# Kernel optimization log

Hardware: AMD Instinct MI355X
Metric: run time of the kernel (lower is better)

Reference implementation:

```python
import jax, jax.numpy as jnp
import numpy as np

B, S, H, F, E = 2, 2048, 1024, 4096, 8  # batch, seq, hidden, ffn, num_experts


def setup_inputs() -> dict:
    key = jax.random.key(0)
    ks = jax.random.split(key, 4)
    x = jax.random.normal(ks[0], (B, S, H), dtype=jnp.float32)
    w_router = jax.random.normal(ks[1], (H, E), dtype=jnp.float32) * 0.02
    w1 = jax.random.normal(ks[2], (E, H, F), dtype=jnp.float32) * 0.02
    b1 = jnp.zeros((E, F), dtype=jnp.float32)
    w2 = jax.random.normal(ks[3], (E, F, H), dtype=jnp.float32) * 0.02
    b2 = jnp.zeros((E, H), dtype=jnp.float32)
    return {"x": x, "w_router": w_router, "w1": w1, "b1": b1, "w2": w2, "b2": b2}


def reference(x, w_router, w1, b1, w2, b2):
    """Top-1 MoE layer: route -> per-expert FFN -> weighted combine.

    Faithful to ExpertParallelWrapper._process_moe_layer on a single group:
    router picks one expert per token with a routing weight; tokens are
    dispatched to experts (here expressed as a static mask over the fixed
    expert set), processed by the expert FFN, and scatter-combined back
    weighted by the routing probability.
    """
    Bs, Ss, Hs = x.shape
    n_experts = w1.shape[0]
    # Router: per-token logits -> softmax -> top-1 expert + weight
    logits = jnp.einsum('bsh,he->bse', x, w_router)          # [B,S,E]
    probs = jax.nn.softmax(logits, axis=-1)
    sel = jnp.argmax(probs, axis=-1)                          # [B,S] selected expert
    wgt = jnp.take_along_axis(probs, sel[..., None], axis=-1)[..., 0]  # [B,S]

    xt = x.reshape(-1, Hs)        # [T,H] flat tokens
    sel_t = sel.reshape(-1)       # [T]
    wgt_t = wgt.reshape(-1)       # [T]

    out = jnp.zeros_like(xt)
    # Static loop over the small fixed expert set (dispatch/combine via mask).
    for e in range(n_experts):
        h = jax.nn.relu(xt @ w1[e] + b1[e])   # [T,F]
        y = h @ w2[e] + b2[e]                 # [T,H]
        m = (sel_t == e).astype(xt.dtype) * wgt_t
        out = out + m[:, None] * y
    return out.reshape(Bs, Ss, Hs)
```

## Files before the change

### kernel.cpp

```cpp
#include <hip/hip_runtime.h>
#include <math.h>

#define T_TOK 4096
#define H_DIM 1024
#define F_DIM 4096
#define E_NUM 8
#define BK 64

typedef __attribute__((ext_vector_type(8))) short bhalf8_t;
typedef __attribute__((ext_vector_type(8))) unsigned short ushort8_t;
typedef __attribute__((ext_vector_type(4))) float f32x4_t;

__device__ __forceinline__ unsigned short f2bf(float f) {
  unsigned int u = __float_as_uint(f);
  return (unsigned short)((u + 0x7fffu + ((u >> 16) & 1u)) >> 16);
}

__device__ __forceinline__ void gload16(const void* g, void* l) {
  __builtin_amdgcn_global_load_lds(
      (const __attribute__((address_space(1))) unsigned int*)g,
      (__attribute__((address_space(3))) unsigned int*)l, 16, 0, 0);
}

__global__ void k_init(int* counts) {
  if (threadIdx.x < E_NUM) counts[threadIdx.x] = 0;
}

__global__ __launch_bounds__(256) void k_router(const float* __restrict__ x,
                                                const float* __restrict__ wr,
                                                int* __restrict__ sel, float* __restrict__ wgt,
                                                int* __restrict__ counts) {
  const int t = blockIdx.x * 4 + (threadIdx.x >> 6);
  const int lane = threadIdx.x & 63;
  const float* xr = x + (size_t)t * H_DIM;
  double acc[E_NUM] = {0, 0, 0, 0, 0, 0, 0, 0};
  for (int h = lane; h < H_DIM; h += 64) {
    const double xv = (double)xr[h];
    const float* w = wr + (size_t)h * E_NUM;
#pragma unroll
    for (int e = 0; e < E_NUM; ++e) acc[e] += xv * (double)w[e];
  }
#pragma unroll
  for (int e = 0; e < E_NUM; ++e) {
#pragma unroll
    for (int off = 32; off > 0; off >>= 1) acc[e] += __shfl_down(acc[e], off, 64);
  }
  if (lane == 0) {
    double m = acc[0];
    int a = 0;
#pragma unroll
    for (int e = 1; e < E_NUM; ++e)
      if (acc[e] > m) { m = acc[e]; a = e; }
    double s = 0.0;
#pragma unroll
    for (int e = 0; e < E_NUM; ++e) s += exp(acc[e] - m);
    sel[t] = a;
    wgt[t] = (float)(1.0 / s);
    atomicAdd(&counts[a], 1);
  }
}

__global__ void k_prefix(const int* __restrict__ counts, int* __restrict__ offs,
                         int* __restrict__ cursors) {
  if (threadIdx.x == 0 && blockIdx.x == 0) {
    int s = 0;
    for (int e = 0; e < E_NUM; ++e) {
      offs[e] = s;
      cursors[e] = s;
      s += counts[e];
    }
    offs[E_NUM] = s;
  }
}

__global__ void k_scatter(const float* __restrict__ x, const int* __restrict__ sel,
                          const float* __restrict__ wgt, int* __restrict__ cursors,
                          int* __restrict__ s2t, float* __restrict__ wgtS,
                          unsigned short* __restrict__ Xs) {
  const int t = blockIdx.x;
  __shared__ int sslot;
  if (threadIdx.x == 0) {
    const int slot = atomicAdd(&cursors[sel[t]], 1);
    sslot = slot;
    s2t[slot] = t;
    wgtS[slot] = wgt[t];
  }
  __syncthreads();
  const int slot = sslot;
  const float4 v = reinterpret_cast<const float4*>(x + (size_t)t * H_DIM)[threadIdx.x];
  ushort4 o;
  o.x = f2bf(v.x); o.y = f2bf(v.y); o.z = f2bf(v.z); o.w = f2bf(v.w);
  reinterpret_cast<ushort4*>(Xs + (size_t)slot * H_DIM)[threadIdx.x] = o;
}

__global__ __launch_bounds__(256) void k_transpose(const float* __restrict__ in,
                                                   unsigned short* __restrict__ out,
                                                   int K, int N) {
  const int e = blockIdx.z;
  const int n0 = blockIdx.x * 64;
  const int k0 = blockIdx.y * 64;
  __shared__ float tile[64][65];
  const float* src = in + (size_t)e * K * N;
  unsigned short* dst = out + (size_t)e * N * K;
  const int l = threadIdx.x;
  const int lr = l >> 4;
  const int lc = (l & 15) * 4;
#pragma unroll
  for (int i = 0; i < 64; i += 16) {
    const float4 v = *reinterpret_cast<const float4*>(&src[(size_t)(k0 + lr + i) * N + n0 + lc]);
    tile[lr + i][lc] = v.x;
    tile[lr + i][lc + 1] = v.y;
    tile[lr + i][lc + 2] = v.z;
    tile[lr + i][lc + 3] = v.w;
  }
  __syncthreads();
  const int kk = (l & 7) * 8;
  const int nr = l >> 3;
#pragma unroll
  for (int i = 0; i < 64; i += 32) {
    const int n = nr + i;
    ushort8_t o;
#pragma unroll
    for (int j = 0; j < 8; ++j) o[j] = f2bf(tile[kk + j][n]);
    *reinterpret_cast<ushort8_t*>(&dst[(size_t)(n0 + n) * K + k0 + kk]) = o;
  }
}

__global__ __launch_bounds__(256, 4) void k_ffn1(const unsigned short* __restrict__ Xs,
                                                 const unsigned short* __restrict__ Wt,
                                                 const float* __restrict__ b1,
                                                 unsigned short* __restrict__ Hws,
                                                 const int* __restrict__ offs) {
  const int e = blockIdx.z;
  const int off = offs[e];
  const int cnt = offs[e + 1] - off;
  const int m0 = blockIdx.y * 128;
  if (m0 >= cnt) return;
  const int n0 = blockIdx.x * 128;
  const int msize = cnt - m0;

  __shared__ short lA[128 * BK];
  __shared__ short lB[128 * BK];

  const int tid = threadIdx.x;
  const int lane = tid & 63;
  const int wv = tid >> 6;
  const int wm = (wv >> 1) * 64;
  const int wn = (wv & 1) * 64;

  const int sRow = lane >> 3;
  const int cc = lane & 7;
  const int gch = cc ^ sRow;

  const unsigned short* Abase = Xs + (size_t)off * H_DIM;
  const unsigned short* Bbase = Wt + (size_t)e * F_DIM * H_DIM + (size_t)n0 * H_DIM;

  f32x4_t acc[4][4];
#pragma unroll
  for (int i = 0; i < 4; ++i)
#pragma unroll
    for (int j = 0; j < 4; ++j) acc[i][j] = (f32x4_t){0.f, 0.f, 0.f, 0.f};

  const int q = lane >> 4;
  const int r16 = lane & 15;
  const int sw = r16 & 7;

  for (int k0 = 0; k0 < H_DIM; k0 += BK) {
    __syncthreads();
#pragma unroll
    for (int i = 0; i < 4; ++i) {
      const int g = wv * 4 + i;
      const int row = g * 8 + sRow;
      const int ar = (row < msize) ? row : 0;
      gload16(Abase + (size_t)(m0 + ar) * H_DIM + k0 + gch * 8, &lA[g * 8 * BK]);
      gload16(Bbase + (size_t)row * H_DIM + k0 + gch * 8, &lB[g * 8 * BK]);
    }
    __syncthreads();

#pragma unroll
    for (int step = 0; step < 2; ++step) {
      const int slot = (step * 4 + q) ^ sw;
      bhalf8_t af[4], bf[4];
#pragma unroll
      for (int mi = 0; mi < 4; ++mi)
        af[mi] = *reinterpret_cast<const bhalf8_t*>(&lA[(wm + mi * 16 + r16) * BK + slot * 8]);
#pragma unroll
      for (int ni = 0; ni < 4; ++ni)
        bf[ni] = *reinterpret_cast<const bhalf8_t*>(&lB[(wn + ni * 16 + r16) * BK + slot * 8]);
#pragma unroll
      for (int mi = 0; mi < 4; ++mi)
#pragma unroll
        for (int ni = 0; ni < 4; ++ni)
          acc[mi][ni] = __builtin_amdgcn_mfma_f32_16x16x32_bf16(af[mi], bf[ni], acc[mi][ni], 0, 0, 0);
    }
  }

  const int c = lane & 15;
#pragma unroll
  for (int ni = 0; ni < 4; ++ni) {
    const int col = n0 + wn + ni * 16 + c;
    const float bias = b1[e * F_DIM + col];
#pragma unroll
    for (int mi = 0; mi < 4; ++mi) {
      const int rbase = wm + mi * 16 + q * 4;
#pragma unroll
      for (int r = 0; r < 4; ++r) {
        const int row = rbase + r;
        if (row < msize) {
          float v = acc[mi][ni][r] + bias;
          v = fmaxf(v, 0.0f);
          Hws[(size_t)(off + m0 + row) * F_DIM + col] = f2bf(v);
        }
      }
    }
  }
}

__global__ __launch_bounds__(256, 4) void k_ffn2(const unsigned short* __restrict__ Hws,
                                                 const unsigned short* __restrict__ Wt,
                                                 const float* __restrict__ b2,
                                                 const int* __restrict__ offs,
                                                 const int* __restrict__ s2t,
                                                 const float* __restrict__ wgtS,
                                                 float* __restrict__ out) {
  const int e = blockIdx.z;
  const int off = offs[e];
  const int cnt = offs[e + 1] - off;
  const int m0 = blockIdx.y * 128;
  if (m0 >= cnt) return;
  const int n0 = blockIdx.x * 128;
  const int msize = cnt - m0;

  __shared__ short lA[128 * BK];
  __shared__ short lB[128 * BK];

  const int tid = threadIdx.x;
  const int lane = tid & 63;
  const int wv = tid >> 6;
  const int wm = (wv >> 1) * 64;
  const int wn = (wv & 1) * 64;

  const int sRow = lane >> 3;
  const int cc = lane & 7;
  const int gch = cc ^ sRow;

  const unsigned short* Abase = Hws + (size_t)off * F_DIM;
  const unsigned short* Bbase = Wt + (size_t)e * H_DIM * F_DIM + (size_t)n0 * F_DIM;

  f32x4_t acc[4][4];
#pragma unroll
  for (int i = 0; i < 4; ++i)
#pragma unroll
    for (int j = 0; j < 4; ++j) acc[i][j] = (f32x4_t){0.f, 0.f, 0.f, 0.f};

  const int q = lane >> 4;
  const int r16 = lane & 15;
  const int sw = r16 & 7;

  for (int k0 = 0; k0 < F_DIM; k0 += BK) {
    __syncthreads();
#pragma unroll
    for (int i = 0; i < 4; ++i) {
      const int g = wv * 4 + i;
      const int row = g * 8 + sRow;
      const int ar = (row < msize) ? row : 0;
      gload16(Abase + (size_t)(m0 + ar) * F_DIM + k0 + gch * 8, &lA[g * 8 * BK]);
      gload16(Bbase + (size_t)row * F_DIM + k0 + gch * 8, &lB[g * 8 * BK]);
    }
    __syncthreads();

#pragma unroll
    for (int step = 0; step < 2; ++step) {
      const int slot = (step * 4 + q) ^ sw;
      bhalf8_t af[4], bf[4];
#pragma unroll
      for (int mi = 0; mi < 4; ++mi)
        af[mi] = *reinterpret_cast<const bhalf8_t*>(&lA[(wm + mi * 16 + r16) * BK + slot * 8]);
#pragma unroll
      for (int ni = 0; ni < 4; ++ni)
        bf[ni] = *reinterpret_cast<const bhalf8_t*>(&lB[(wn + ni * 16 + r16) * BK + slot * 8]);
#pragma unroll
      for (int mi = 0; mi < 4; ++mi)
#pragma unroll
        for (int ni = 0; ni < 4; ++ni)
          acc[mi][ni] = __builtin_amdgcn_mfma_f32_16x16x32_bf16(af[mi], bf[ni], acc[mi][ni], 0, 0, 0);
    }
  }

  const int c = lane & 15;
#pragma unroll
  for (int mi = 0; mi < 4; ++mi) {
    const int rbase = wm + mi * 16 + q * 4;
#pragma unroll
    for (int r = 0; r < 4; ++r) {
      const int row = rbase + r;
      if (row >= msize) continue;
      const int srow = off + m0 + row;
      const int tok = s2t[srow];
      const float w = wgtS[srow];
      float* orow = out + (size_t)tok * H_DIM;
#pragma unroll
      for (int ni = 0; ni < 4; ++ni) {
        const int col = n0 + wn + ni * 16 + c;
        orow[col] = w * (acc[mi][ni][r] + b2[e * H_DIM + col]);
      }
    }
  }
}

extern "C" void kernel_launch(void* const* d_in, const int* in_sizes, int n_in,
                              void* d_out, int out_size, void* d_ws, size_t ws_size,
                              hipStream_t stream) {
  const float* x  = (const float*)d_in[0];
  const float* wr = (const float*)d_in[1];
  const float* w1 = (const float*)d_in[2];
  const float* b1 = (const float*)d_in[3];
  const float* w2 = (const float*)d_in[4];
  const float* b2 = (const float*)d_in[5];
  float* out = (float*)d_out;

  char* ws = (char*)d_ws;
  unsigned short* WT  = (unsigned short*)(ws);
  unsigned short* XS  = (unsigned short*)(ws + 67108864);
  unsigned short* HWS = (unsigned short*)(ws + 67108864 + 8388608);
  char* ctrl = ws + 67108864 + 8388608 + 33554432;
  int*   sel     = (int*)(ctrl);
  int*   s2t     = (int*)(ctrl + 16384);
  float* wgt     = (float*)(ctrl + 32768);
  float* wgtS    = (float*)(ctrl + 49152);
  int*   counts  = (int*)(ctrl + 65536);
  int*   offs    = (int*)(ctrl + 65536 + 64);
  int*   cursors = (int*)(ctrl + 65536 + 128);

  k_init<<<1, 64, 0, stream>>>(counts);
  k_router<<<T_TOK / 4, 256, 0, stream>>>(x, wr, sel, wgt, counts);
  k_prefix<<<1, 1, 0, stream>>>(counts, offs, cursors);
  k_scatter<<<T_TOK, 256, 0, stream>>>(x, sel, wgt, cursors, s2t, wgtS, XS);

  k_transpose<<<dim3(F_DIM / 64, H_DIM / 64, E_NUM), 256, 0, stream>>>(w1, WT, H_DIM, F_DIM);
  k_ffn1<<<dim3(F_DIM / 128, T_TOK / 128, E_NUM), 256, 0, stream>>>(XS, WT, b1, HWS, offs);

  k_transpose<<<dim3(H_DIM / 64, F_DIM / 64, E_NUM), 256, 0, stream>>>(w2, WT, F_DIM, H_DIM);
  k_ffn2<<<dim3(H_DIM / 128, T_TOK / 128, E_NUM), 256, 0, stream>>>(HWS, WT, b2, offs, s2t, wgtS, out);
}
```

Before: 579.9 us.

## Split-K the second expert GEMM and narrow FFN1 tiles for more blocks

The second expert GEMM is split four ways along the F dimension. Each split writes fp32 partial sums to a workspace buffer, and a new reduce kernel adds them, applies bias and routing weight, and scatters rows back to token order. The first GEMM's N tile drops from 128 to 64 to double block count. Both changes aim to fill the GPU better when per-expert token counts are small. The cost is extra global traffic for partials plus a reduce launch, and lower arithmetic intensity per FFN1 block. Split-K runs only when the workspace is large enough.

Result: faster. 551.9 us (-4.8%).

```diff
diff --git a/kernel.cpp b/kernel.cpp
--- a/kernel.cpp
+++ b/kernel.cpp
@@ -6,6 +6,7 @@
 #define F_DIM 4096
 #define E_NUM 8
 #define BK 64
+#define KSPLIT 4
 
 typedef __attribute__((ext_vector_type(8))) short bhalf8_t;
 typedef __attribute__((ext_vector_type(8))) unsigned short ushort8_t;
@@ -76,14 +77,16 @@
 __global__ void k_scatter(const float* __restrict__ x, const int* __restrict__ sel,
                           const float* __restrict__ wgt, int* __restrict__ cursors,
                           int* __restrict__ s2t, float* __restrict__ wgtS,
-                          unsigned short* __restrict__ Xs) {
+                          int* __restrict__ eS, unsigned short* __restrict__ Xs) {
   const int t = blockIdx.x;
   __shared__ int sslot;
   if (threadIdx.x == 0) {
-    const int slot = atomicAdd(&cursors[sel[t]], 1);
+    const int e = sel[t];
+    const int slot = atomicAdd(&cursors[e], 1);
     sslot = slot;
     s2t[slot] = t;
     wgtS[slot] = wgt[t];
+    eS[slot] = e;
   }
   __syncthreads();
   const int slot = sslot;
@@ -136,17 +139,17 @@
   const int cnt = offs[e + 1] - off;
   const int m0 = blockIdx.y * 128;
   if (m0 >= cnt) return;
-  const int n0 = blockIdx.x * 128;
+  const int n0 = blockIdx.x * 64;
   const int msize = cnt - m0;
 
   __shared__ short lA[128 * BK];
-  __shared__ short lB[128 * BK];
+  __shared__ short lB[64 * BK];
 
   const int tid = threadIdx.x;
   const int lane = tid & 63;
   const int wv = tid >> 6;
   const int wm = (wv >> 1) * 64;
-  const int wn = (wv & 1) * 64;
+  const int wn = (wv & 1) * 32;
 
   const int sRow = lane >> 3;
   const int cc = lane & 7;
@@ -155,11 +158,11 @@
   const unsigned short* Abase = Xs + (size_t)off * H_DIM;
   const unsigned short* Bbase = Wt + (size_t)e * F_DIM * H_DIM + (size_t)n0 * H_DIM;
 
-  f32x4_t acc[4][4];
+  f32x4_t acc[4][2];
 #pragma unroll
   for (int i = 0; i < 4; ++i)
 #pragma unroll
-    for (int j = 0; j < 4; ++j) acc[i][j] = (f32x4_t){0.f, 0.f, 0.f, 0.f};
+    for (int j = 0; j < 2; ++j) acc[i][j] = (f32x4_t){0.f, 0.f, 0.f, 0.f};
 
   const int q = lane >> 4;
   const int r16 = lane & 15;
@@ -173,6 +176,11 @@
       const int row = g * 8 + sRow;
       const int ar = (row < msize) ? row : 0;
       gload16(Abase + (size_t)(m0 + ar) * H_DIM + k0 + gch * 8, &lA[g * 8 * BK]);
+    }
+#pragma unroll
+    for (int i = 0; i < 2; ++i) {
+      const int g = wv * 2 + i;
+      const int row = g * 8 + sRow;
       gload16(Bbase + (size_t)row * H_DIM + k0 + gch * 8, &lB[g * 8 * BK]);
     }
     __syncthreads();
@@ -180,24 +188,24 @@
 #pragma unroll
     for (int step = 0; step < 2; ++step) {
       const int slot = (step * 4 + q) ^ sw;
-      bhalf8_t af[4], bf[4];
+      bhalf8_t af[4], bf[2];
 #pragma unroll
       for (int mi = 0; mi < 4; ++mi)
         af[mi] = *reinterpret_cast<const bhalf8_t*>(&lA[(wm + mi * 16 + r16) * BK + slot * 8]);
 #pragma unroll
-      for (int ni = 0; ni < 4; ++ni)
+      for (int ni = 0; ni < 2; ++ni)
         bf[ni] = *reinterpret_cast<const bhalf8_t*>(&lB[(wn + ni * 16 + r16) * BK + slot * 8]);
 #pragma unroll
       for (int mi = 0; mi < 4; ++mi)
 #pragma unroll
-        for (int ni = 0; ni < 4; ++ni)
+        for (int ni = 0; ni < 2; ++ni)
           acc[mi][ni] = __builtin_amdgcn_mfma_f32_16x16x32_bf16(af[mi], bf[ni], acc[mi][ni], 0, 0, 0);
     }
   }
 
   const int c = lane & 15;
 #pragma unroll
-  for (int ni = 0; ni < 4; ++ni) {
+  for (int ni = 0; ni < 2; ++ni) {
     const int col = n0 + wn + ni * 16 + c;
     const float bias = b1[e * F_DIM + col];
 #pragma unroll
@@ -216,13 +224,125 @@
   }
 }
 
-__global__ __launch_bounds__(256, 4) void k_ffn2(const unsigned short* __restrict__ Hws,
-                                                 const unsigned short* __restrict__ Wt,
-                                                 const float* __restrict__ b2,
-                                                 const int* __restrict__ offs,
-                                                 const int* __restrict__ s2t,
-                                                 const float* __restrict__ wgtS,
-                                                 float* __restrict__ out) {
+__global__ __launch_bounds__(256, 4) void k_ffn2_sk(const unsigned short* __restrict__ Hws,
+                                                    const unsigned short* __restrict__ Wt,
+                                                    const int* __restrict__ offs,
+                                                    float* __restrict__ P) {
+  const int e = blockIdx.z >> 2;
+  const int ks = blockIdx.z & 3;
+  const int off = offs[e];
+  const int cnt = offs[e + 1] - off;
+  const int m0 = blockIdx.y * 128;
+  if (m0 >= cnt) return;
+  const int n0 = blockIdx.x * 128;
+  const int msize = cnt - m0;
+  const int kbeg = ks * (F_DIM / KSPLIT);
+  const int kend = kbeg + (F_DIM / KSPLIT);
+
+  __shared__ short lA[128 * BK];
+  __shared__ short lB[128 * BK];
+
+  const int tid = threadIdx.x;
+  const int lane = tid & 63;
+  const int wv = tid >> 6;
+  const int wm = (wv >> 1) * 64;
+  const int wn = (wv & 1) * 64;
+
+  const int sRow = lane >> 3;
+  const int cc = lane & 7;
+  const int gch = cc ^ sRow;
+
+  const unsigned short* Abase = Hws + (size_t)off * F_DIM;
+  const unsigned short* Bbase = Wt + (size_t)e * H_DIM * F_DIM + (size_t)n0 * F_DIM;
+
+  f32x4_t acc[4][4];
+#pragma unroll
+  for (int i = 0; i < 4; ++i)
+#pragma unroll
+    for (int j = 0; j < 4; ++j) acc[i][j] = (f32x4_t){0.f, 0.f, 0.f, 0.f};
+
+  const int q = lane >> 4;
+  const int r16 = lane & 15;
+  const int sw = r16 & 7;
+
+  for (int k0 = kbeg; k0 < kend; k0 += BK) {
+    __syncthreads();
+#pragma unroll
+    for (int i = 0; i < 4; ++i) {
+      const int g = wv * 4 + i;
+      const int row = g * 8 + sRow;
+      const int ar = (row < msize) ? row : 0;
+      gload16(Abase + (size_t)(m0 + ar) * F_DIM + k0 + gch * 8, &lA[g * 8 * BK]);
+      gload16(Bbase + (size_t)row * F_DIM + k0 + gch * 8, &lB[g * 8 * BK]);
+    }
+    __syncthreads();
+
+#pragma unroll
+    for (int step = 0; step < 2; ++step) {
+      const int slot = (step * 4 + q) ^ sw;
+      bhalf8_t af[4], bf[4];
+#pragma unroll
+      for (int mi = 0; mi < 4; ++mi)
+        af[mi] = *reinterpret_cast<const bhalf8_t*>(&lA[(wm + mi * 16 + r16) * BK + slot * 8]);
+#pragma unroll
+      for (int ni = 0; ni < 4; ++ni)
+        bf[ni] = *reinterpret_cast<const bhalf8_t*>(&lB[(wn + ni * 16 + r16) * BK + slot * 8]);
+#pragma unroll
+      for (int mi = 0; mi < 4; ++mi)
+#pragma unroll
+        for (int ni = 0; ni < 4; ++ni)
+          acc[mi][ni] = __builtin_amdgcn_mfma_f32_16x16x32_bf16(af[mi], bf[ni], acc[mi][ni], 0, 0, 0);
+    }
+  }
+
+  const int c = lane & 15;
+  float* Pb = P + (size_t)ks * T_TOK * H_DIM;
+#pragma unroll
+  for (int mi = 0; mi < 4; ++mi) {
+    const int rbase = wm + mi * 16 + q * 4;
+#pragma unroll
+    for (int r = 0; r < 4; ++r) {
+      const int row = rbase + r;
+      if (row >= msize) continue;
+      float* prow = Pb + (size_t)(off + m0 + row) * H_DIM;
+#pragma unroll
+      for (int ni = 0; ni < 4; ++ni) prow[n0 + wn + ni * 16 + c] = acc[mi][ni][r];
+    }
+  }
+}
+
+__global__ __launch_bounds__(256) void k_reduce(const float* __restrict__ P,
+                                                const float* __restrict__ b2,
+                                                const int* __restrict__ s2t,
+                                                const int* __restrict__ eS,
+                                                const float* __restrict__ wgtS,
+                                                float* __restrict__ out) {
+  const int srow = blockIdx.x;
+  const int tok = s2t[srow];
+  const int e = eS[srow];
+  const float w = wgtS[srow];
+  const int i = threadIdx.x;
+  const size_t rowoff = (size_t)srow * H_DIM / 4 + i;
+  const float4 p0 = reinterpret_cast<const float4*>(P)[rowoff];
+  const float4 p1 = reinterpret_cast<const float4*>(P + (size_t)T_TOK * H_DIM)[rowoff];
+  const float4 p2 = reinterpret_cast<const float4*>(P + (size_t)2 * T_TOK * H_DIM)[rowoff];
+  const float4 p3 = reinterpret_cast<const float4*>(P + (size_t)3 * T_TOK * H_DIM)[rowoff];
+  const float4 b = reinterpret_cast<const float4*>(b2 + (size_t)e * H_DIM)[i];
+  float4 o;
+  o.x = w * (p0.x + p1.x + p2.x + p3.x + b.x);
+  o.y = w * (p0.y + p1.y + p2.y + p3.y + b.y);
+  o.z = w * (p0.z + p1.z + p2.z + p3.z + b.z);
+  o.w = w * (p0.w + p1.w + p2.w + p3.w + b.w);
+  reinterpret_cast<float4*>(out + (size_t)tok * H_DIM)[i] = o;
+}
+
+__global__ __launch_bounds__(256, 4) void k_ffn2_direct(const unsigned short* __restrict__ Hws,
+                                                        const unsigned short* __restrict__ Wt,
+                                                        const float* __restrict__ b2,
+                                                        const int* __restrict__ offs,
+                                                        const int* __restrict__ s2t,
+                                                        const float* __restrict__ wgtS,
+                                                        float* __restrict__ out) {
   const int e = blockIdx.z;
   const int off = offs[e];
   const int cnt = offs[e + 1] - off;
@@ -323,23 +443,31 @@
   unsigned short* WT  = (unsigned short*)(ws);
   unsigned short* XS  = (unsigned short*)(ws + 67108864);
   unsigned short* HWS = (unsigned short*)(ws + 67108864 + 8388608);
-  char* ctrl = ws + 67108864 + 8388608 + 33554432;
+  char* ctrl = ws + 109051904;
   int*   sel     = (int*)(ctrl);
   int*   s2t     = (int*)(ctrl + 16384);
   float* wgt     = (float*)(ctrl + 32768);
   float* wgtS    = (float*)(ctrl + 49152);
-  int*   counts  = (int*)(ctrl + 65536);
-  int*   offs    = (int*)(ctrl + 65536 + 64);
-  int*   cursors = (int*)(ctrl + 65536 + 128);
+  int*   eS      = (int*)(ctrl + 65536);
+  int*   counts  = (int*)(ctrl + 81920);
+  int*   offs    = (int*)(ctrl + 81920 + 64);
+  int*   cursors = (int*)(ctrl + 81920 + 128);
+  float* P = (float*)(ws + 109150208);
+  const bool use_splitk = ws_size >= (size_t)(109150208) + (size_t)KSPLIT * T_TOK * H_DIM * 4;
 
   k_init<<<1, 64, 0, stream>>>(counts);
   k_router<<<T_TOK / 4, 256, 0, stream>>>(x, wr, sel, wgt, counts);
   k_prefix<<<1, 1, 0, stream>>>(counts, offs, cursors);
-  k_scatter<<<T_TOK, 256, 0, stream>>>(x, sel, wgt, cursors, s2t, wgtS, XS);
+  k_scatter<<<T_TOK, 256, 0, stream>>>(x, sel, wgt, cursors, s2t, wgtS, eS, XS);
 
   k_transpose<<<dim3(F_DIM / 64, H_DIM / 64, E_NUM), 256, 0, stream>>>(w1, WT, H_DIM, F_DIM);
-  k_ffn1<<<dim3(F_DIM / 128, T_TOK / 128, E_NUM), 256, 0, stream>>>(XS, WT, b1, HWS, offs);
+  k_ffn1<<<dim3(F_DIM / 64, T_TOK / 128, E_NUM), 256, 0, stream>>>(XS, WT, b1, HWS, offs);
 
   k_transpose<<<dim3(H_DIM / 64, F_DIM / 64, E_NUM), 256, 0, stream>>>(w2, WT, F_DIM, H_DIM);
-  k_ffn2<<<dim3(H_DIM / 128, T_TOK / 128, E_NUM), 256, 0, stream>>>(HWS, WT, b2, offs, s2t, wgtS, out);
-}
+  if (use_splitk) {
+    k_ffn2_sk<<<dim3(H_DIM / 128, T_TOK / 128, E_NUM * KSPLIT), 256, 0, stream>>>(HWS, WT, offs, P);
+    k_reduce<<<T_TOK, 256, 0, stream>>>(P, b2, s2t, eS, wgtS, out);
+  } else {
+    k_ffn2_direct<<<dim3(H_DIM / 128, T_TOK / 128, E_NUM), 256, 0, stream>>>(HWS, WT, b2, offs, s2t, wgtS, out);
+  }
+}
```
